# Optimization experiments

Measured on AMD Instinct MI355X. Metric: run time of the kernel, lower is better.

## Reference

```python
import jax, jax.numpy as jnp
import numpy as np

N_NODES = 100000


def gcn_conv(x, edge_index, W, b):
    """PyG-style GCNConv: x' = D^-1/2 (A+I) D^-1/2 (x W) + b (self-loops added)."""
    n = x.shape[0]
    h = x @ W  # [N, out]
    loop = jnp.arange(n, dtype=edge_index.dtype)
    src = jnp.concatenate([edge_index[0], loop])  # [E+N]
    dst = jnp.concatenate([edge_index[1], loop])
    deg = jax.ops.segment_sum(jnp.ones_like(dst, dtype=h.dtype), dst, num_segments=n)
    dinv = jnp.where(deg > 0, jax.lax.rsqrt(deg), 0.0)
    norm = dinv[src] * dinv[dst]  # [E+N]
    # gather -> scale -> scatter-add aggregation
    out = jax.ops.segment_sum(norm[:, None] * h[src], dst, num_segments=n)
    return out + b


def setup_inputs() -> dict:
    key = jax.random.key(0)
    k1, k2, k3, k4 = jax.random.split(key, 4)
    n, e = N_NODES, 2560000
    x = jax.random.normal(k1, (n, 2), dtype=jnp.float32)
    edge_index = jax.random.randint(k2, (2, e), 0, n, dtype=jnp.int32)
    hidden = 32
    W1 = jax.random.normal(k3, (2, hidden), dtype=jnp.float32) * (1.0 / np.sqrt(2))
    b1 = jnp.zeros((hidden,), dtype=jnp.float32)
    W2 = jax.random.normal(k4, (hidden, 1), dtype=jnp.float32) * (1.0 / np.sqrt(hidden))
    b2 = jnp.zeros((1,), dtype=jnp.float32)
    return {"x": x, "edge_index": edge_index, "W1": W1, "b1": b1, "W2": W2, "b2": b2}


def reference(x, edge_index, W1, b1, W2, b2):
    h = jax.nn.relu(gcn_conv(x, edge_index, W1, b1))
    return gcn_conv(h, edge_index, W2, b2)  # [N, 1]
```

## Files before the change

kernel.cpp:

```cpp
#include <hip/hip_runtime.h>


#define NR 32
#define RS_MAX 3200
#define AGG_BLKS 16
#define CHUNK 4096
#define DBITS 12
#define DMASK 4095


__global__ void k_px(const float2* __restrict__ x, const int* __restrict__ pdeg,
                     float* __restrict__ dinv, float2* __restrict__ px, int n) {
    int i = blockIdx.x * blockDim.x + threadIdx.x;
    if (i >= n) return;
    int deg = 1;
#pragma unroll
    for (int b = 0; b < AGG_BLKS; ++b) deg += pdeg[b * n + i];
    float d = rsqrtf((float)deg);
    dinv[i] = d;
    float2 xv = x[i];
    px[i] = make_float2(d * xv.x, d * xv.y);
}

__global__ void k_node(const float2* __restrict__ px, const float2* __restrict__ pP,
                       const float* __restrict__ dinv,
                       const float* __restrict__ W1, const float* __restrict__ b1,
                       const float* __restrict__ W2, float* __restrict__ s, int n) {
    int i = blockIdx.x * blockDim.x + threadIdx.x;
    if (i >= n) return;
    float2 v = px[i];
    float ax = v.x, ay = v.y;
#pragma unroll
    for (int b = 0; b < AGG_BLKS; ++b) {
        float2 p = pP[b * n + i];
        ax += p.x; ay += p.y;
    }
    float d = dinv[i];
    float dot = 0.f;
#pragma unroll
    for (int j = 0; j < 32; ++j) {
        float acc = fmaf(ax, W1[j], ay * W1[32 + j]);
        float h = fmaxf(fmaf(d, acc, b1[j]), 0.f);
        dot = fmaf(h, W2[j], dot);
    }
    s[i] = d * dot;
}

__global__ void k_out(const float* __restrict__ s, const float* __restrict__ ps,
                      const float* __restrict__ dinv, const float* __restrict__ b2,
                      float* __restrict__ out, int n) {
    int i = blockIdx.x * blockDim.x + threadIdx.x;
    if (i >= n) return;
    float acc = s[i];
#pragma unroll
    for (int b = 0; b < AGG_BLKS; ++b) acc += ps[b * n + i];
    out[i] = dinv[i] * acc + b2[0];
}


__global__ void k_bcount(const int* __restrict__ dst, int* __restrict__ btot,
                         int e, int rs) {
    __shared__ int h[NR];
    if (threadIdx.x < NR) h[threadIdx.x] = 0;
    __syncthreads();
    int eq = e >> 2;
    const int4* d4 = (const int4*)dst;
    for (int i = blockIdx.x * blockDim.x + threadIdx.x; i < eq; i += gridDim.x * blockDim.x) {
        int4 v = d4[i];
        atomicAdd(&h[v.x / rs], 1);
        atomicAdd(&h[v.y / rs], 1);
        atomicAdd(&h[v.z / rs], 1);
        atomicAdd(&h[v.w / rs], 1);
    }
    if (blockIdx.x == 0 && threadIdx.x == 0)
        for (int i = eq * 4; i < e; ++i) atomicAdd(&h[dst[i] / rs], 1);
    __syncthreads();
    if (threadIdx.x < NR) atomicAdd(&btot[threadIdx.x * 16], h[threadIdx.x]);
}

__global__ void k_bscan(const int* __restrict__ btot, int* __restrict__ bstart,
                        int* __restrict__ bcnt, int* __restrict__ bcur) {
    if (threadIdx.x == 0 && blockIdx.x == 0) {
        int acc = 0;
        for (int r = 0; r < NR; ++r) {
            int c = btot[r * 16];
            bstart[r] = acc; bcnt[r] = c; bcur[r * 16] = acc;
            acc += (c + 3) & ~3;
        }
    }
}

__global__ void k_bscatter(const int* __restrict__ src, const int* __restrict__ dst,
                           int* __restrict__ bcur, unsigned* __restrict__ packed,
                           int e, int rs) {
    __shared__ int h[NR], cur[NR];
    int c0 = blockIdx.x * CHUNK;
    int c1 = min(c0 + CHUNK, e);
    if (threadIdx.x < NR) h[threadIdx.x] = 0;
    __syncthreads();
    const int4* d4 = (const int4*)dst;
    const int4* s4 = (const int4*)src;
    for (int i = c0 + threadIdx.x * 4; i < c1; i += blockDim.x * 4) {
        if (i + 4 <= c1) {
            int4 v = d4[i >> 2];
            atomicAdd(&h[v.x / rs], 1);
            atomicAdd(&h[v.y / rs], 1);
            atomicAdd(&h[v.z / rs], 1);
            atomicAdd(&h[v.w / rs], 1);
        } else {
            for (int j = i; j < c1; ++j) atomicAdd(&h[dst[j] / rs], 1);
        }
    }
    __syncthreads();
    if (threadIdx.x < NR)
        cur[threadIdx.x] = atomicAdd(&bcur[threadIdx.x * 16], h[threadIdx.x]);
    __syncthreads();
    for (int i = c0 + threadIdx.x * 4; i < c1; i += blockDim.x * 4) {
        if (i + 4 <= c1) {
            int4 dv = d4[i >> 2];
            int4 sv = s4[i >> 2];
            int r0 = dv.x / rs; int t0 = atomicAdd(&cur[r0], 1);
            packed[t0] = ((unsigned)sv.x << DBITS) | (unsigned)(dv.x - r0 * rs);
            int r1 = dv.y / rs; int t1 = atomicAdd(&cur[r1], 1);
            packed[t1] = ((unsigned)sv.y << DBITS) | (unsigned)(dv.y - r1 * rs);
            int r2 = dv.z / rs; int t2 = atomicAdd(&cur[r2], 1);
            packed[t2] = ((unsigned)sv.z << DBITS) | (unsigned)(dv.z - r2 * rs);
            int r3 = dv.w / rs; int t3 = atomicAdd(&cur[r3], 1);
            packed[t3] = ((unsigned)sv.w << DBITS) | (unsigned)(dv.w - r3 * rs);
        } else {
            for (int j = i; j < c1; ++j) {
                int d = dst[j];
                int r = d / rs;
                int slot = atomicAdd(&cur[r], 1);
                packed[slot] = ((unsigned)src[j] << DBITS) | (unsigned)(d - r * rs);
            }
        }
    }
}


__global__ __launch_bounds__(1024, 8)
void k_deg(const unsigned* __restrict__ packed, const int* __restrict__ bstart,
           const int* __restrict__ bcnt, int* __restrict__ pdeg, int rs, int n) {
    __shared__ int acc[RS_MAX];
    int r = blockIdx.y, b = blockIdx.x;
    int rs_r = min(rs, n - r * rs);
    for (int t = threadIdx.x; t < rs_r; t += blockDim.x) acc[t] = 0;
    __syncthreads();
    int c = bcnt[r], base = bstart[r];
    int q = (c + 3) >> 2;
    int qper = (q + gridDim.x - 1) / gridDim.x;
    int qlo = b * qper, qhi = min(qlo + qper, q);
    const uint4* p4 = (const uint4*)(packed + base);
    for (int j = qlo + threadIdx.x; j < qhi; j += blockDim.x) {
        uint4 v = p4[j];
        int lim = c - j * 4;
        atomicAdd(&acc[v.x & DMASK], 1);
        if (lim > 1) atomicAdd(&acc[v.y & DMASK], 1);
        if (lim > 2) atomicAdd(&acc[v.z & DMASK], 1);
        if (lim > 3) atomicAdd(&acc[v.w & DMASK], 1);
    }
    __syncthreads();
    int nb = b * n + r * rs;
    for (int t = threadIdx.x; t < rs_r; t += blockDim.x) pdeg[nb + t] = acc[t];
}

__global__ __launch_bounds__(1024, 8)
void k_agg1(const unsigned* __restrict__ packed, const int* __restrict__ bstart,
            const int* __restrict__ bcnt, const float2* __restrict__ px,
            float2* __restrict__ pP, int rs, int n) {
    __shared__ float acc[2 * RS_MAX];
    int r = blockIdx.y, b = blockIdx.x;
    int rs_r = min(rs, n - r * rs);
    for (int t = threadIdx.x; t < 2 * rs_r; t += blockDim.x) acc[t] = 0.f;
    __syncthreads();
    int c = bcnt[r], base = bstart[r];
    int q = (c + 3) >> 2;
    int qper = (q + gridDim.x - 1) / gridDim.x;
    int qlo = b * qper, qhi = min(qlo + qper, q);
    const uint4* p4 = (const uint4*)(packed + base);
    int nm1 = n - 1;
    for (int j = qlo + threadIdx.x; j < qhi; j += blockDim.x) {
        uint4 v = p4[j];
        int i0 = (int)(v.x >> DBITS);
        int i1 = min((int)(v.y >> DBITS), nm1);
        int i2 = min((int)(v.z >> DBITS), nm1);
        int i3 = min((int)(v.w >> DBITS), nm1);
        float2 g0 = px[i0], g1 = px[i1], g2 = px[i2], g3 = px[i3];
        int lim = c - j * 4;
        int d0 = (v.x & DMASK) * 2;
        atomicAdd(&acc[d0], g0.x); atomicAdd(&acc[d0 + 1], g0.y);
        if (lim > 1) { int d1 = (v.y & DMASK) * 2; atomicAdd(&acc[d1], g1.x); atomicAdd(&acc[d1 + 1], g1.y); }
        if (lim > 2) { int d2 = (v.z & DMASK) * 2; atomicAdd(&acc[d2], g2.x); atomicAdd(&acc[d2 + 1], g2.y); }
        if (lim > 3) { int d3 = (v.w & DMASK) * 2; atomicAdd(&acc[d3], g3.x); atomicAdd(&acc[d3 + 1], g3.y); }
    }
    __syncthreads();
    int nb = b * n + r * rs;
    for (int t = threadIdx.x; t < rs_r; t += blockDim.x)
        pP[nb + t] = make_float2(acc[2 * t], acc[2 * t + 1]);
}

__global__ __launch_bounds__(1024, 8)
void k_agg2(const unsigned* __restrict__ packed, const int* __restrict__ bstart,
            const int* __restrict__ bcnt, const float* __restrict__ s,
            float* __restrict__ ps, int rs, int n) {
    __shared__ float acc[RS_MAX];
    int r = blockIdx.y, b = blockIdx.x;
    int rs_r = min(rs, n - r * rs);
    for (int t = threadIdx.x; t < rs_r; t += blockDim.x) acc[t] = 0.f;
    __syncthreads();
    int c = bcnt[r], base = bstart[r];
    int q = (c + 3) >> 2;
    int qper = (q + gridDim.x - 1) / gridDim.x;
    int qlo = b * qper, qhi = min(qlo + qper, q);
    const uint4* p4 = (const uint4*)(packed + base);
    int nm1 = n - 1;
    for (int j = qlo + threadIdx.x; j < qhi; j += blockDim.x) {
        uint4 v = p4[j];
        int i0 = (int)(v.x >> DBITS);
        int i1 = min((int)(v.y >> DBITS), nm1);
        int i2 = min((int)(v.z >> DBITS), nm1);
        int i3 = min((int)(v.w >> DBITS), nm1);
        float g0 = s[i0], g1 = s[i1], g2 = s[i2], g3 = s[i3];
        int lim = c - j * 4;
        atomicAdd(&acc[v.x & DMASK], g0);
        if (lim > 1) atomicAdd(&acc[v.y & DMASK], g1);
        if (lim > 2) atomicAdd(&acc[v.z & DMASK], g2);
        if (lim > 3) atomicAdd(&acc[v.w & DMASK], g3);
    }
    __syncthreads();
    int nb = b * n + r * rs;
    for (int t = threadIdx.x; t < rs_r; t += blockDim.x) ps[nb + t] = acc[t];
}


__global__ void f_zero(int* __restrict__ ideg, float2* __restrict__ P, int n) {
    int i = blockIdx.x * blockDim.x + threadIdx.x;
    if (i < n) { ideg[i] = 0; P[i] = make_float2(0.f, 0.f); }
}
__global__ void f_count(const int* __restrict__ dst, int* __restrict__ ideg, int e) {
    int i = blockIdx.x * blockDim.x + threadIdx.x;
    if (i < e) atomicAdd(&ideg[dst[i]], 1);
}
__global__ void f_px(const float2* __restrict__ x, const int* __restrict__ ideg,
                     float* __restrict__ dinv, float2* __restrict__ px, int n) {
    int i = blockIdx.x * blockDim.x + threadIdx.x;
    if (i >= n) return;
    float d = rsqrtf((float)(1 + ideg[i]));
    dinv[i] = d;
    float2 xv = x[i];
    px[i] = make_float2(d * xv.x, d * xv.y);
}
__global__ void f_scatter_px(const int* __restrict__ src, const int* __restrict__ dst,
                             const float2* __restrict__ px, float* __restrict__ Pf, int e) {
    int i = blockIdx.x * blockDim.x + threadIdx.x;
    if (i >= e) return;
    int sidx = src[i], d = dst[i];
    float2 v = px[sidx];
    atomicAdd(&Pf[2 * d], v.x);
    atomicAdd(&Pf[2 * d + 1], v.y);
}
__global__ void f_node(const float2* __restrict__ px, const float2* __restrict__ P,
                       const float* __restrict__ dinv,
                       const float* __restrict__ W1, const float* __restrict__ b1,
                       const float* __restrict__ W2,
                       float* __restrict__ s, float* __restrict__ S, int n) {
    int i = blockIdx.x * blockDim.x + threadIdx.x;
    if (i >= n) return;
    float d = dinv[i];
    float2 v = px[i], p = P[i];
    float ax = v.x + p.x, ay = v.y + p.y;
    float dot = 0.f;
#pragma unroll
    for (int j = 0; j < 32; ++j) {
        float acc = fmaf(ax, W1[j], ay * W1[32 + j]);
        float h = fmaxf(fmaf(d, acc, b1[j]), 0.f);
        dot = fmaf(h, W2[j], dot);
    }
    float sv = d * dot;
    s[i] = sv;
    S[i] = sv;
}
__global__ void f_scatter_s(const int* __restrict__ src, const int* __restrict__ dst,
                            const float* __restrict__ s, float* __restrict__ S, int e) {
    int i = blockIdx.x * blockDim.x + threadIdx.x;
    if (i < e) atomicAdd(&S[dst[i]], s[src[i]]);
}
__global__ void f_out(const float* __restrict__ S, const float* __restrict__ dinv,
                      const float* __restrict__ b2, float* __restrict__ out, int n) {
    int i = blockIdx.x * blockDim.x + threadIdx.x;
    if (i < n) out[i] = dinv[i] * S[i] + b2[0];
}


extern "C" void kernel_launch(void* const* d_in, const int* in_sizes, int n_in,
                              void* d_out, int out_size, void* d_ws, size_t ws_size,
                              hipStream_t stream) {
    const float* x  = (const float*)d_in[0];
    const int*   ei = (const int*)d_in[1];
    const float* W1 = (const float*)d_in[2];
    const float* b1 = (const float*)d_in[3];
    const float* W2 = (const float*)d_in[4];
    const float* b2 = (const float*)d_in[5];
    float* out = (float*)d_out;

    int n = in_sizes[0] / 2;
    int e = in_sizes[1] / 2;
    const int* src = ei;
    const int* dst = ei + e;
    int rs = (n + NR - 1) / NR;

    char* ws = (char*)d_ws;
    auto align = [](size_t v) { return (v + 255) & ~(size_t)255; };
    size_t off = 0;
    float*  dinv = (float*) (ws + off); off = align(off + (size_t)n * 4);
    float2* px   = (float2*)(ws + off); off = align(off + (size_t)n * 8);
    float*  s    = (float*) (ws + off); off = align(off + (size_t)n * 4);
    int*    pdeg = (int*)   (ws + off); off = align(off + (size_t)AGG_BLKS * n * 4);
    float2* pP   = (float2*)(ws + off); off = align(off + (size_t)AGG_BLKS * n * 8);
    float*  ps   = (float*) (ws + off); off = align(off + (size_t)AGG_BLKS * n * 4);
    int*    bstart = (int*)(ws + off); off = align(off + NR * 4);
    int*    bcnt   = (int*)(ws + off); off = align(off + NR * 4);
    int*    btot   = (int*)(ws + off);
    int*    bcur   = btot + NR * 16;   off = align(off + (size_t)NR * 16 * 2 * 4);
    unsigned* packed = (unsigned*)(ws + off);
    size_t need = off + (size_t)(e + 4 * NR) * 4;

    const int B = 256;
    int gn = (n + B - 1) / B, ge = (e + B - 1) / B;

    bool fast = (need <= ws_size) && (rs <= RS_MAX) && (rs <= DMASK + 1) &&
                (n <= (1 << (31 - DBITS)));

    if (fast) {
        dim3 ag(AGG_BLKS, NR);
        hipMemsetAsync(btot, 0, (size_t)NR * 16 * 2 * 4, stream);
        k_bcount  <<<256, B, 0, stream>>>(dst, btot, e, rs);
        k_bscan   <<<1, 64, 0, stream>>>(btot, bstart, bcnt, bcur);
        k_bscatter<<<(e + CHUNK - 1) / CHUNK, B, 0, stream>>>(src, dst, bcur, packed, e, rs);
        k_deg     <<<ag, 1024, 0, stream>>>(packed, bstart, bcnt, pdeg, rs, n);
        k_px      <<<gn, B, 0, stream>>>((const float2*)x, pdeg, dinv, px, n);
        k_agg1    <<<ag, 1024, 0, stream>>>(packed, bstart, bcnt, px, pP, rs, n);
        k_node    <<<gn, B, 0, stream>>>(px, pP, dinv, W1, b1, W2, s, n);
        k_agg2    <<<ag, 1024, 0, stream>>>(packed, bstart, bcnt, s, ps, rs, n);
        k_out     <<<gn, B, 0, stream>>>(s, ps, dinv, b2, out, n);
    } else {
        int*   ideg = pdeg;
        float2* P   = pP;
        float* S    = ps;
        f_zero      <<<gn, B, 0, stream>>>(ideg, P, n);
        f_count     <<<ge, B, 0, stream>>>(dst, ideg, e);
        f_px        <<<gn, B, 0, stream>>>((const float2*)x, ideg, dinv, px, n);
        f_scatter_px<<<ge, B, 0, stream>>>(src, dst, px, (float*)P, e);
        f_node      <<<gn, B, 0, stream>>>(px, P, dinv, W1, b1, W2, s, S, n);
        f_scatter_s <<<ge, B, 0, stream>>>(src, dst, s, S, e);
        f_out       <<<gn, B, 0, stream>>>(S, dinv, b2, out, n);
    }
}
```

Measured before the change: 107.1 us.

## Stage bucket scatter in shared memory and fuse bucket scan into count kernel

The scatter kernel now sorts each chunk of edges into its buckets in LDS and then writes each bucket contiguously to global memory, replacing random per-edge global writes with coalesced runs. The separate single-thread scan kernel is folded into the count kernel using a last-block-done atomic counter. Bucket size becomes a fixed power of two (4096), so divisions by the bucket size become shifts and masks. The cost is extra LDS use in the scatter kernel and a serial loop over buckets when copying out, and the bucket count now depends on n (25 for this input) instead of a fixed 32.

```diff
diff --git a/kernel.cpp b/kernel.cpp
--- a/kernel.cpp
+++ b/kernel.cpp
@@ -1,8 +1,7 @@
 #include <hip/hip_runtime.h>
 
 
-#define NR 32
-#define RS_MAX 3200
+#define NRMAX 32
 #define AGG_BLKS 16
 #define CHUNK 4096
 #define DBITS 12
@@ -59,92 +58,109 @@
 
 
 __global__ void k_bcount(const int* __restrict__ dst, int* __restrict__ btot,
-                         int e, int rs) {
-    __shared__ int h[NR];
-    if (threadIdx.x < NR) h[threadIdx.x] = 0;
+                         int* __restrict__ done, int* __restrict__ bstart,
+                         int* __restrict__ bcnt, int* __restrict__ bcur,
+                         int e, int NR) {
+    __shared__ int h[NRMAX];
+    if (threadIdx.x < NRMAX) h[threadIdx.x] = 0;
     __syncthreads();
     int eq = e >> 2;
     const int4* d4 = (const int4*)dst;
     for (int i = blockIdx.x * blockDim.x + threadIdx.x; i < eq; i += gridDim.x * blockDim.x) {
         int4 v = d4[i];
-        atomicAdd(&h[v.x / rs], 1);
-        atomicAdd(&h[v.y / rs], 1);
-        atomicAdd(&h[v.z / rs], 1);
-        atomicAdd(&h[v.w / rs], 1);
+        atomicAdd(&h[v.x >> DBITS], 1);
+        atomicAdd(&h[v.y >> DBITS], 1);
+        atomicAdd(&h[v.z >> DBITS], 1);
+        atomicAdd(&h[v.w >> DBITS], 1);
     }
     if (blockIdx.x == 0 && threadIdx.x == 0)
-        for (int i = eq * 4; i < e; ++i) atomicAdd(&h[dst[i] / rs], 1);
-    __syncthreads();
-    if (threadIdx.x < NR) atomicAdd(&btot[threadIdx.x * 16], h[threadIdx.x]);
-}
-
-__global__ void k_bscan(const int* __restrict__ btot, int* __restrict__ bstart,
-                        int* __restrict__ bcnt, int* __restrict__ bcur) {
-    if (threadIdx.x == 0 && blockIdx.x == 0) {
-        int acc = 0;
-        for (int r = 0; r < NR; ++r) {
-            int c = btot[r * 16];
-            bstart[r] = acc; bcnt[r] = c; bcur[r * 16] = acc;
-            acc += (c + 3) & ~3;
+        for (int i = eq * 4; i < e; ++i) atomicAdd(&h[dst[i] >> DBITS], 1);
+    __syncthreads();
+    if (threadIdx.x < NR && h[threadIdx.x])
+        atomicAdd(&btot[threadIdx.x * 16], h[threadIdx.x]);
+    __threadfence();
+    __syncthreads();
+    if (threadIdx.x == 0) {
+        int t = atomicAdd(done, 1);
+        if (t == (int)gridDim.x - 1) {
+            int acc = 0;
+            for (int r = 0; r < NR; ++r) {
+                int c = atomicAdd(&btot[r * 16], 0);
+                bstart[r] = acc; bcnt[r] = c; bcur[r * 16] = acc;
+                acc += (c + 3) & ~3;
+            }
         }
     }
 }
 
 __global__ void k_bscatter(const int* __restrict__ src, const int* __restrict__ dst,
                            int* __restrict__ bcur, unsigned* __restrict__ packed,
-                           int e, int rs) {
-    __shared__ int h[NR], cur[NR];
+                           int e, int NR) {
+    __shared__ int h[NRMAX], lofs[NRMAX], gbase[NRMAX], cur[NRMAX];
+    __shared__ unsigned sbuf[CHUNK];
     int c0 = blockIdx.x * CHUNK;
     int c1 = min(c0 + CHUNK, e);
-    if (threadIdx.x < NR) h[threadIdx.x] = 0;
-    __syncthreads();
-    const int4* d4 = (const int4*)dst;
-    const int4* s4 = (const int4*)src;
-    for (int i = c0 + threadIdx.x * 4; i < c1; i += blockDim.x * 4) {
-        if (i + 4 <= c1) {
-            int4 v = d4[i >> 2];
-            atomicAdd(&h[v.x / rs], 1);
-            atomicAdd(&h[v.y / rs], 1);
-            atomicAdd(&h[v.z / rs], 1);
-            atomicAdd(&h[v.w / rs], 1);
-        } else {
-            for (int j = i; j < c1; ++j) atomicAdd(&h[dst[j] / rs], 1);
+    if (threadIdx.x < NRMAX) h[threadIdx.x] = 0;
+    __syncthreads();
+    const int4* d4 = (const int4*)(dst + c0);
+    const int4* s4 = (const int4*)(src + c0);
+    int len = c1 - c0;
+    int lq = len >> 2;
+    for (int j = threadIdx.x; j < lq; j += blockDim.x) {
+        int4 v = d4[j];
+        atomicAdd(&h[v.x >> DBITS], 1);
+        atomicAdd(&h[v.y >> DBITS], 1);
+        atomicAdd(&h[v.z >> DBITS], 1);
+        atomicAdd(&h[v.w >> DBITS], 1);
+    }
+    if (threadIdx.x == 0)
+        for (int i = lq * 4; i < len; ++i) atomicAdd(&h[dst[c0 + i] >> DBITS], 1);
+    __syncthreads();
+    if (threadIdx.x == 0) {
+        int acc = 0;
+        for (int r = 0; r < NR; ++r) { lofs[r] = acc; acc += h[r]; }
+    }
+    __syncthreads();
+    if (threadIdx.x < NR) {
+        cur[threadIdx.x] = lofs[threadIdx.x];
+        if (h[threadIdx.x] > 0)
+            gbase[threadIdx.x] = atomicAdd(&bcur[threadIdx.x * 16], h[threadIdx.x]);
+    }
+    __syncthreads();
+    for (int j = threadIdx.x; j < lq; j += blockDim.x) {
+        int4 dv = d4[j];
+        int4 sv = s4[j];
+        int r0 = dv.x >> DBITS; int t0 = atomicAdd(&cur[r0], 1);
+        sbuf[t0] = ((unsigned)sv.x << DBITS) | (unsigned)(dv.x & DMASK);
+        int r1 = dv.y >> DBITS; int t1 = atomicAdd(&cur[r1], 1);
+        sbuf[t1] = ((unsigned)sv.y << DBITS) | (unsigned)(dv.y & DMASK);
+        int r2 = dv.z >> DBITS; int t2 = atomicAdd(&cur[r2], 1);
+        sbuf[t2] = ((unsigned)sv.z << DBITS) | (unsigned)(dv.z & DMASK);
+        int r3 = dv.w >> DBITS; int t3 = atomicAdd(&cur[r3], 1);
+        sbuf[t3] = ((unsigned)sv.w << DBITS) | (unsigned)(dv.w & DMASK);
+    }
+    if (threadIdx.x == 0)
+        for (int i = lq * 4; i < len; ++i) {
+            int d = dst[c0 + i];
+            int r = d >> DBITS;
+            int t = atomicAdd(&cur[r], 1);
+            sbuf[t] = ((unsigned)src[c0 + i] << DBITS) | (unsigned)(d & DMASK);
         }
-    }
-    __syncthreads();
-    if (threadIdx.x < NR)
-        cur[threadIdx.x] = atomicAdd(&bcur[threadIdx.x * 16], h[threadIdx.x]);
-    __syncthreads();
-    for (int i = c0 + threadIdx.x * 4; i < c1; i += blockDim.x * 4) {
-        if (i + 4 <= c1) {
-            int4 dv = d4[i >> 2];
-            int4 sv = s4[i >> 2];
-            int r0 = dv.x / rs; int t0 = atomicAdd(&cur[r0], 1);
-            packed[t0] = ((unsigned)sv.x << DBITS) | (unsigned)(dv.x - r0 * rs);
-            int r1 = dv.y / rs; int t1 = atomicAdd(&cur[r1], 1);
-            packed[t1] = ((unsigned)sv.y << DBITS) | (unsigned)(dv.y - r1 * rs);
-            int r2 = dv.z / rs; int t2 = atomicAdd(&cur[r2], 1);
-            packed[t2] = ((unsigned)sv.z << DBITS) | (unsigned)(dv.z - r2 * rs);
-            int r3 = dv.w / rs; int t3 = atomicAdd(&cur[r3], 1);
-            packed[t3] = ((unsigned)sv.w << DBITS) | (unsigned)(dv.w - r3 * rs);
-        } else {
-            for (int j = i; j < c1; ++j) {
-                int d = dst[j];
-                int r = d / rs;
-                int slot = atomicAdd(&cur[r], 1);
-                packed[slot] = ((unsigned)src[j] << DBITS) | (unsigned)(d - r * rs);
-            }
-        }
+    __syncthreads();
+    for (int r = 0; r < NR; ++r) {
+        int cnt = h[r], lo = lofs[r], gb = gbase[r];
+        for (int t = threadIdx.x; t < cnt; t += blockDim.x)
+            packed[gb + t] = sbuf[lo + t];
     }
 }
 
 
 __global__ __launch_bounds__(1024, 8)
 void k_deg(const unsigned* __restrict__ packed, const int* __restrict__ bstart,
-           const int* __restrict__ bcnt, int* __restrict__ pdeg, int rs, int n) {
-    __shared__ int acc[RS_MAX];
+           const int* __restrict__ bcnt, int* __restrict__ pdeg, int n) {
+    __shared__ int acc[DMASK + 1];
     int r = blockIdx.y, b = blockIdx.x;
-    int rs_r = min(rs, n - r * rs);
+    int rs_r = min(DMASK + 1, n - (r << DBITS));
     for (int t = threadIdx.x; t < rs_r; t += blockDim.x) acc[t] = 0;
     __syncthreads();
     int c = bcnt[r], base = bstart[r];
@@ -161,17 +177,17 @@
         if (lim > 3) atomicAdd(&acc[v.w & DMASK], 1);
     }
     __syncthreads();
-    int nb = b * n + r * rs;
+    int nb = b * n + (r << DBITS);
     for (int t = threadIdx.x; t < rs_r; t += blockDim.x) pdeg[nb + t] = acc[t];
 }
 
 __global__ __launch_bounds__(1024, 8)
 void k_agg1(const unsigned* __restrict__ packed, const int* __restrict__ bstart,
             const int* __restrict__ bcnt, const float2* __restrict__ px,
-            float2* __restrict__ pP, int rs, int n) {
-    __shared__ float acc[2 * RS_MAX];
+            float2* __restrict__ pP, int n) {
+    __shared__ float acc[2 * (DMASK + 1)];
     int r = blockIdx.y, b = blockIdx.x;
-    int rs_r = min(rs, n - r * rs);
+    int rs_r = min(DMASK + 1, n - (r << DBITS));
     for (int t = threadIdx.x; t < 2 * rs_r; t += blockDim.x) acc[t] = 0.f;
     __syncthreads();
     int c = bcnt[r], base = bstart[r];
@@ -195,7 +211,7 @@
         if (lim > 3) { int d3 = (v.w & DMASK) * 2; atomicAdd(&acc[d3], g3.x); atomicAdd(&acc[d3 + 1], g3.y); }
     }
     __syncthreads();
-    int nb = b * n + r * rs;
+    int nb = b * n + (r << DBITS);
     for (int t = threadIdx.x; t < rs_r; t += blockDim.x)
         pP[nb + t] = make_float2(acc[2 * t], acc[2 * t + 1]);
 }
@@ -203,10 +219,10 @@
 __global__ __launch_bounds__(1024, 8)
 void k_agg2(const unsigned* __restrict__ packed, const int* __restrict__ bstart,
             const int* __restrict__ bcnt, const float* __restrict__ s,
-            float* __restrict__ ps, int rs, int n) {
-    __shared__ float acc[RS_MAX];
+            float* __restrict__ ps, int n) {
+    __shared__ float acc[DMASK + 1];
     int r = blockIdx.y, b = blockIdx.x;
-    int rs_r = min(rs, n - r * rs);
+    int rs_r = min(DMASK + 1, n - (r << DBITS));
     for (int t = threadIdx.x; t < rs_r; t += blockDim.x) acc[t] = 0.f;
     __syncthreads();
     int c = bcnt[r], base = bstart[r];
@@ -229,7 +245,7 @@
         if (lim > 3) atomicAdd(&acc[v.w & DMASK], g3);
     }
     __syncthreads();
-    int nb = b * n + r * rs;
+    int nb = b * n + (r << DBITS);
     for (int t = threadIdx.x; t < rs_r; t += blockDim.x) ps[nb + t] = acc[t];
 }
 
@@ -308,7 +324,7 @@
     int e = in_sizes[1] / 2;
     const int* src = ei;
     const int* dst = ei + e;
-    int rs = (n + NR - 1) / NR;
+    int NR = (n + DMASK) >> DBITS;
 
     char* ws = (char*)d_ws;
     auto align = [](size_t v) { return (v + 255) & ~(size_t)255; };
@@ -319,30 +335,31 @@
     int*    pdeg = (int*)   (ws + off); off = align(off + (size_t)AGG_BLKS * n * 4);
     float2* pP   = (float2*)(ws + off); off = align(off + (size_t)AGG_BLKS * n * 8);
     float*  ps   = (float*) (ws + off); off = align(off + (size_t)AGG_BLKS * n * 4);
-    int*    bstart = (int*)(ws + off); off = align(off + NR * 4);
-    int*    bcnt   = (int*)(ws + off); off = align(off + NR * 4);
+    int*    bstart = (int*)(ws + off); off = align(off + NRMAX * 4);
+    int*    bcnt   = (int*)(ws + off); off = align(off + NRMAX * 4);
     int*    btot   = (int*)(ws + off);
-    int*    bcur   = btot + NR * 16;   off = align(off + (size_t)NR * 16 * 2 * 4);
+    int*    bcur   = btot + NRMAX * 16;
+    int*    done   = bcur + NRMAX * 16;
+    size_t  ctrl_bytes = (size_t)(NRMAX * 16 * 2 + 16) * 4;
+    off = align(off + ctrl_bytes);
     unsigned* packed = (unsigned*)(ws + off);
-    size_t need = off + (size_t)(e + 4 * NR) * 4;
+    size_t need = off + (size_t)(e + 4 * NRMAX) * 4;
 
     const int B = 256;
     int gn = (n + B - 1) / B, ge = (e + B - 1) / B;
 
-    bool fast = (need <= ws_size) && (rs <= RS_MAX) && (rs <= DMASK + 1) &&
-                (n <= (1 << (31 - DBITS)));
+    bool fast = (need <= ws_size) && (NR <= NRMAX) && (n <= (1 << 17));
 
     if (fast) {
         dim3 ag(AGG_BLKS, NR);
-        hipMemsetAsync(btot, 0, (size_t)NR * 16 * 2 * 4, stream);
-        k_bcount  <<<256, B, 0, stream>>>(dst, btot, e, rs);
-        k_bscan   <<<1, 64, 0, stream>>>(btot, bstart, bcnt, bcur);
-        k_bscatter<<<(e + CHUNK - 1) / CHUNK, B, 0, stream>>>(src, dst, bcur, packed, e, rs);
-        k_deg     <<<ag, 1024, 0, stream>>>(packed, bstart, bcnt, pdeg, rs, n);
+        hipMemsetAsync(btot, 0, ctrl_bytes, stream);
+        k_bcount  <<<512, B, 0, stream>>>(dst, btot, done, bstart, bcnt, bcur, e, NR);
+        k_bscatter<<<(e + CHUNK - 1) / CHUNK, B, 0, stream>>>(src, dst, bcur, packed, e, NR);
+        k_deg     <<<ag, 1024, 0, stream>>>(packed, bstart, bcnt, pdeg, n);
         k_px      <<<gn, B, 0, stream>>>((const float2*)x, pdeg, dinv, px, n);
-        k_agg1    <<<ag, 1024, 0, stream>>>(packed, bstart, bcnt, px, pP, rs, n);
+        k_agg1    <<<ag, 1024, 0, stream>>>(packed, bstart, bcnt, px, pP, n);
         k_node    <<<gn, B, 0, stream>>>(px, pP, dinv, W1, b1, W2, s, n);
-        k_agg2    <<<ag, 1024, 0, stream>>>(packed, bstart, bcnt, s, ps, rs, n);
+        k_agg2    <<<ag, 1024, 0, stream>>>(packed, bstart, bcnt, s, ps, n);
         k_out     <<<gn, B, 0, stream>>>(s, ps, dinv, b2, out, n);
     } else {
         int*   ideg = pdeg;
```

Result: slower. 147.6 us (+37.8%).
